# Kernel optimization log

Measured on AMD Instinct MI355X. Metric: run time of the kernel, lower is better.

## Reference

```python
import jax, jax.numpy as jnp
import numpy as np

B, S, H, NH, HD, L, I, M = 2, 2048, 768, 12, 64, 6, 3072, 256
VOCAB, TYPES = 30522, 2
EPS = 1e-6  # layernorm epsilon and FAVOR+ numerical stabilizer


def layer_norm(x, g, b):
    mu = jnp.mean(x, axis=-1, keepdims=True)
    var = jnp.mean(jax.lax.square(x), axis=-1, keepdims=True) - jax.lax.square(mu)
    return (x - mu) * jax.lax.rsqrt(var + EPS) * g + b


def favor_attention(q, k, v, mask, proj):
    # q,k,v: [B,S,NH,HD]; proj: [M,HD] random features; mask: [B,S] float
    dn = 1.0 / np.sqrt(np.sqrt(HD))      # data normalizer for softmax kernel
    ratio = 1.0 / np.sqrt(M)
    qn, kn = q * dn, k * dn
    qp = jnp.einsum('bsnd,md->bsnm', qn, proj)
    kp = jnp.einsum('bsnd,md->bsnm', kn, proj)
    qd = 0.5 * jnp.sum(qn * qn, axis=-1, keepdims=True)
    kd = 0.5 * jnp.sum(kn * kn, axis=-1, keepdims=True)
    # stabilizers: per-position max for queries, global (seq+feature) max for keys
    q_prime = ratio * (jnp.exp(qp - qd - jnp.max(qp, axis=-1, keepdims=True)) + EPS)
    k_prime = ratio * (jnp.exp(kp - kd - jnp.max(kp, axis=(1, 3), keepdims=True)) + EPS)
    k_prime = k_prime * mask[:, :, None, None]
    kv = jnp.einsum('bsnm,bsnd->bnmd', k_prime, v)          # [B,NH,M,HD]
    num = jnp.einsum('bsnm,bnmd->bsnd', q_prime, kv)        # [B,S,NH,HD]
    den = jnp.einsum('bsnm,bnm->bsn', q_prime, jnp.sum(k_prime, axis=1))
    return num / den[..., None]


def setup_inputs() -> dict:
    key = jax.random.key(0)
    ks = jax.random.split(key, 32)
    f = lambda i, shape, s=0.02: (jax.random.normal(ks[i], shape, jnp.float32) * s)
    inp = {
        'input_ids': jax.random.randint(ks[0], (B, S), 0, VOCAB, jnp.int32),
        'token_type_ids': jax.random.randint(ks[1], (B, S), 0, TYPES, jnp.int32),
        'position_ids': jnp.tile(jnp.arange(S, dtype=jnp.int32)[None, :], (B, 1)),
        'attention_mask': jnp.ones((B, S), jnp.int32),
        'word_emb': f(2, (VOCAB, H), 0.1),
        'pos_emb': f(3, (S, H), 0.1),
        'type_emb': f(4, (TYPES, H), 0.1),
        'emb_ln_g': jnp.ones((H,), jnp.float32),
        'emb_ln_b': jnp.zeros((H,), jnp.float32),
        'wq': f(5, (L, H, NH, HD)), 'bq': jnp.zeros((L, NH, HD), jnp.float32),
        'wk': f(6, (L, H, NH, HD)), 'bk': jnp.zeros((L, NH, HD), jnp.float32),
        'wv': f(7, (L, H, NH, HD)), 'bv': jnp.zeros((L, NH, HD), jnp.float32),
        'wo': f(8, (L, NH, HD, H)), 'bo': jnp.zeros((L, H), jnp.float32),
        'ln1_g': jnp.ones((L, H), jnp.float32), 'ln1_b': jnp.zeros((L, H), jnp.float32),
        'wi': f(9, (L, H, I)), 'bi': jnp.zeros((L, I), jnp.float32),
        'wo2': f(10, (L, I, H)), 'bo2': jnp.zeros((L, H), jnp.float32),
        'ln2_g': jnp.ones((L, H), jnp.float32), 'ln2_b': jnp.zeros((L, H), jnp.float32),
        'proj': jax.random.normal(ks[11], (L, M, HD), jnp.float32),
    }
    return inp


def reference(input_ids, token_type_ids, position_ids, attention_mask,
              word_emb, pos_emb, type_emb, emb_ln_g, emb_ln_b,
              wq, bq, wk, bk, wv, bv, wo, bo, ln1_g, ln1_b,
              wi, bi, wo2, bo2, ln2_g, ln2_b, proj):
    mask = attention_mask.astype(jnp.float32)
    x = word_emb[input_ids] + pos_emb[position_ids] + type_emb[token_type_ids]
    x = layer_norm(x, emb_ln_g, emb_ln_b)
    for l in range(L):
        q = jnp.einsum('bsh,hnd->bsnd', x, wq[l]) + bq[l]
        k = jnp.einsum('bsh,hnd->bsnd', x, wk[l]) + bk[l]
        v = jnp.einsum('bsh,hnd->bsnd', x, wv[l]) + bv[l]
        att = favor_attention(q, k, v, mask, proj[l])
        att = jnp.einsum('bsnd,ndh->bsh', att, wo[l]) + bo[l]
        a = layer_norm(att + x, ln1_g[l], ln1_b[l])
        inter = jax.nn.gelu(jnp.einsum('bsh,hi->bsi', a, wi[l]) + bi[l])
        out = jnp.einsum('bsi,ih->bsh', inter, wo2[l]) + bo2[l]
        x = layer_norm(out + a, ln2_g[l], ln2_b[l])
    return x
```

## Files before the change

kernel.cpp:

```cpp
#include <hip/hip_runtime.h>
#include <hip/hip_bf16.h>

#define B_ 2
#define S_ 2048
#define H_ 768
#define NH_ 12
#define HD_ 64
#define L_ 6
#define I_ 3072
#define M_ 256
#define BS_ 4096
#define R_ 49152
#define NXH_ 3145728
#define EPS_ 1e-6f
#define DN_ 0.35355339059327373f
#define RATIO_ 0.0625f

typedef __attribute__((ext_vector_type(8))) short bf16x8;
typedef __attribute__((ext_vector_type(4))) float f32x4;

__device__ __forceinline__ void gload16(const void* g, void* l) {
    __builtin_amdgcn_global_load_lds(
        (const __attribute__((address_space(1))) void*)g,
        (__attribute__((address_space(3))) void*)l, 16, 0, 0);
}

__device__ __forceinline__ float gelu_f(float x) {
    const float c = 0.7978845608028654f;
    float x3 = x * x * x;
    return 0.5f * x * (1.0f + tanhf(c * (x + 0.044715f * x3)));
}

__device__ __forceinline__ void blockReduceSum2(float& a, float& b) {
    __shared__ float sa[4], sb[4];
    int lane = threadIdx.x & 63, wid = threadIdx.x >> 6;
    #pragma unroll
    for (int off = 32; off; off >>= 1) {
        a += __shfl_down(a, off, 64);
        b += __shfl_down(b, off, 64);
    }
    __syncthreads();
    if (lane == 0) { sa[wid] = a; sb[wid] = b; }
    __syncthreads();
    a = sa[0] + sa[1] + sa[2] + sa[3];
    b = sb[0] + sb[1] + sb[2] + sb[3];
    __syncthreads();
}

__device__ __forceinline__ float blockReduceMax(float v) {
    __shared__ float sm[4];
    int lane = threadIdx.x & 63, wid = threadIdx.x >> 6;
    #pragma unroll
    for (int off = 32; off; off >>= 1) v = fmaxf(v, __shfl_down(v, off, 64));
    __syncthreads();
    if (lane == 0) sm[wid] = v;
    __syncthreads();
    float r = fmaxf(fmaxf(sm[0], sm[1]), fmaxf(sm[2], sm[3]));
    __syncthreads();
    return r;
}

__device__ __forceinline__ float blockReduceSum(float v) {
    __shared__ float sm[4];
    int lane = threadIdx.x & 63, wid = threadIdx.x >> 6;
    #pragma unroll
    for (int off = 32; off; off >>= 1) v += __shfl_down(v, off, 64);
    __syncthreads();
    if (lane == 0) sm[wid] = v;
    __syncthreads();
    float r = sm[0] + sm[1] + sm[2] + sm[3];
    __syncthreads();
    return r;
}

template<int ACT, int OUTMODE>
__global__ __launch_bounds__(256) void gemm_pipe3_kernel(
    const __hip_bfloat16* __restrict__ A, const __hip_bfloat16* __restrict__ BT,
    const float* __restrict__ bias, void* __restrict__ Cv,
    int K, int lda, int ldb, int ldc)
{
    __shared__ __align__(16) unsigned short As[3][128][32];
    __shared__ __align__(16) unsigned short Bs[3][128][32];
    const int tid = threadIdx.x, lane = tid & 63, wid = tid >> 6;
    const int wr = wid >> 1, wc = wid & 1;
    const size_t r0 = (size_t)blockIdx.y * 128;
    const int n0 = blockIdx.x * 128;

    const int srow = lane >> 2;
    const int selem = ((lane & 3) ^ ((srow >> 1) & 3)) * 8;
    const unsigned short* ga0 = (const unsigned short*)A + (r0 + wid * 32 + srow) * (size_t)lda + selem;
    const unsigned short* gb0 = (const unsigned short*)BT + ((size_t)n0 + wid * 32 + srow) * (size_t)ldb + selem;

    f32x4 acc[4][4];
    #pragma unroll
    for (int i = 0; i < 4; i++)
        #pragma unroll
        for (int j = 0; j < 4; j++)
            acc[i][j] = (f32x4){0.f, 0.f, 0.f, 0.f};

    const int lr = lane & 15;
    const int rc8 = (((lane >> 4) ^ ((lr >> 1) & 3))) * 8;

#define STAGE_(t) { const int bb_ = (t) % 3; const int kk_ = (t) * 32;            \
    gload16(ga0 + kk_, &As[bb_][wid * 32][0]);                                    \
    gload16(ga0 + kk_ + 16 * (size_t)lda, &As[bb_][wid * 32 + 16][0]);            \
    gload16(gb0 + kk_, &Bs[bb_][wid * 32][0]);                                    \
    gload16(gb0 + kk_ + 16 * (size_t)ldb, &Bs[bb_][wid * 32 + 16][0]); }

#define ITER_(t, VMSTR, DOSTAGE) {                                                \
    if (DOSTAGE) STAGE_((t) + 2);                                                 \
    asm volatile("s_waitcnt vmcnt(" VMSTR ")" ::: "memory");                      \
    __builtin_amdgcn_sched_barrier(0);                                            \
    __builtin_amdgcn_s_barrier();                                                 \
    __builtin_amdgcn_sched_barrier(0);                                            \
    const int bb_ = (t) % 3;                                                      \
    bf16x8 af[4], bfv[4];                                                         \
    _Pragma("unroll") for (int i = 0; i < 4; i++)                                 \
        af[i] = *(const bf16x8*)&As[bb_][wr * 64 + i * 16 + lr][rc8];             \
    _Pragma("unroll") for (int j = 0; j < 4; j++)                                 \
        bfv[j] = *(const bf16x8*)&Bs[bb_][wc * 64 + j * 16 + lr][rc8];            \
    __builtin_amdgcn_s_setprio(1);                                                \
    _Pragma("unroll") for (int i = 0; i < 4; i++)                                 \
        _Pragma("unroll") for (int j = 0; j < 4; j++)                             \
            acc[i][j] = __builtin_amdgcn_mfma_f32_16x16x32_bf16(af[i], bfv[j], acc[i][j], 0, 0, 0); \
    __builtin_amdgcn_s_setprio(0);                                                \
    __builtin_amdgcn_s_barrier();                                                 \
    __builtin_amdgcn_sched_barrier(0); }

    const int nT = K >> 5;
    STAGE_(0); STAGE_(1);
    for (int t = 0; t < nT - 2; ++t) ITER_(t, "8", true);
    ITER_(nT - 2, "4", false);
    ITER_(nT - 1, "0", false);
#undef ITER_
#undef STAGE_

    const int rr = (lane >> 4) * 4;
    const int cc = lane & 15;
    const size_t seg = (size_t)n0 / 768;
    const int colbase = n0 - (int)seg * 768;
    #pragma unroll
    for (int i = 0; i < 4; i++) {
        #pragma unroll
        for (int j = 0; j < 4; j++) {
            int colw = wc * 64 + j * 16 + cc;
            size_t col = (size_t)n0 + colw;
            float bv_ = bias ? bias[col] : 0.f;
            #pragma unroll
            for (int rg = 0; rg < 4; rg++) {
                size_t row = r0 + wr * 64 + i * 16 + rr + rg;
                float v = acc[i][j][rg] + bv_;
                if (ACT == 1) v = gelu_f(v);
                if (OUTMODE == 1)
                    ((__hip_bfloat16*)Cv)[row * (size_t)ldc + col] = __float2bfloat16(v);
                else
                    ((__hip_bfloat16*)Cv)[seg * (size_t)NXH_ + row * 768 + colbase + colw]
                        = __float2bfloat16(v);
            }
        }
    }
}

__global__ __launch_bounds__(256) void gemm_pipe3_n64_kernel(
    const __hip_bfloat16* __restrict__ A, const __hip_bfloat16* __restrict__ BT,
    const float* __restrict__ bias, float* __restrict__ C,
    int K, int lda, int ldb, int ldc)
{
    __shared__ __align__(16) unsigned short As[3][128][32];
    __shared__ __align__(16) unsigned short Bs[3][64][32];
    const int tid = threadIdx.x, lane = tid & 63, wid = tid >> 6;
    const size_t r0 = (size_t)blockIdx.y * 128;
    const int n0 = blockIdx.x * 64;

    const int srow = lane >> 2;
    const int selem = ((lane & 3) ^ ((srow >> 1) & 3)) * 8;
    const unsigned short* ga0 = (const unsigned short*)A + (r0 + wid * 32 + srow) * (size_t)lda + selem;
    const unsigned short* gb0 = (const unsigned short*)BT + ((size_t)n0 + wid * 16 + srow) * (size_t)ldb + selem;

    f32x4 acc[2][4];
    #pragma unroll
    for (int i = 0; i < 2; i++)
        #pragma unroll
        for (int j = 0; j < 4; j++)
            acc[i][j] = (f32x4){0.f, 0.f, 0.f, 0.f};

    const int lr = lane & 15;
    const int rc8 = (((lane >> 4) ^ ((lr >> 1) & 3))) * 8;

#define STAGE_(t) { const int bb_ = (t) % 3; const int kk_ = (t) * 32;            \
    gload16(ga0 + kk_, &As[bb_][wid * 32][0]);                                    \
    gload16(ga0 + kk_ + 16 * (size_t)lda, &As[bb_][wid * 32 + 16][0]);            \
    gload16(gb0 + kk_, &Bs[bb_][wid * 16][0]); }

#define ITER_(t, VMSTR, DOSTAGE) {                                                \
    if (DOSTAGE) STAGE_((t) + 2);                                                 \
    asm volatile("s_waitcnt vmcnt(" VMSTR ")" ::: "memory");                      \
    __builtin_amdgcn_sched_barrier(0);                                            \
    __builtin_amdgcn_s_barrier();                                                 \
    __builtin_amdgcn_sched_barrier(0);                                            \
    const int bb_ = (t) % 3;                                                      \
    bf16x8 af[2], bfv[4];                                                         \
    _Pragma("unroll") for (int i = 0; i < 2; i++)                                 \
        af[i] = *(const bf16x8*)&As[bb_][wid * 32 + i * 16 + lr][rc8];            \
    _Pragma("unroll") for (int j = 0; j < 4; j++)                                 \
        bfv[j] = *(const bf16x8*)&Bs[bb_][j * 16 + lr][rc8];                      \
    __builtin_amdgcn_s_setprio(1);                                                \
    _Pragma("unroll") for (int i = 0; i < 2; i++)                                 \
        _Pragma("unroll") for (int j = 0; j < 4; j++)                             \
            acc[i][j] = __builtin_amdgcn_mfma_f32_16x16x32_bf16(af[i], bfv[j], acc[i][j], 0, 0, 0); \
    __builtin_amdgcn_s_setprio(0);                                                \
    __builtin_amdgcn_s_barrier();                                                 \
    __builtin_amdgcn_sched_barrier(0); }

    const int nT = K >> 5;
    STAGE_(0); STAGE_(1);
    for (int t = 0; t < nT - 2; ++t) ITER_(t, "6", true);
    ITER_(nT - 2, "3", false);
    ITER_(nT - 1, "0", false);
#undef ITER_
#undef STAGE_

    const int rr = (lane >> 4) * 4, cc = lane & 15;
    #pragma unroll
    for (int i = 0; i < 2; i++) {
        #pragma unroll
        for (int j = 0; j < 4; j++) {
            int col = n0 + j * 16 + cc;
            float bv_ = bias ? bias[col] : 0.f;
            #pragma unroll
            for (int rg = 0; rg < 4; rg++) {
                size_t row = r0 + wid * 32 + i * 16 + rr + rg;
                C[row * (size_t)ldc + col] = acc[i][j][rg] + bv_;
            }
        }
    }
}

template<int RMAXOUT>
__global__ __launch_bounds__(256) void gemm_mfma_kernel(
    const __hip_bfloat16* __restrict__ A, const __hip_bfloat16* __restrict__ BT,
    void* __restrict__ Cv,
    int N, int K, int lda, int ldb, int ldc, float alpha,
    float* __restrict__ rmaxp)
{
    __shared__ __align__(16) unsigned short As[2][128][32];
    __shared__ __align__(16) unsigned short Bs[2][128][32];
    __shared__ float rmx[128][2];
    const int tid = threadIdx.x, lane = tid & 63, wid = tid >> 6;
    const int wr = wid >> 1, wc = wid & 1;
    const size_t r0 = (size_t)blockIdx.y * 128;
    const int n0 = blockIdx.x * 128;

    const int srow = lane >> 2;
    const int selem = ((lane & 3) ^ ((srow >> 1) & 3)) * 8;
    const unsigned short* ga0 = (const unsigned short*)A + (r0 + wid * 32 + srow) * (size_t)lda + selem;
    const unsigned short* gb0 = (const unsigned short*)BT + ((size_t)n0 + wid * 32 + srow) * (size_t)ldb + selem;

    f32x4 acc[4][4];
    #pragma unroll
    for (int i = 0; i < 4; i++)
        #pragma unroll
        for (int j = 0; j < 4; j++)
            acc[i][j] = (f32x4){0.f, 0.f, 0.f, 0.f};

    gload16(ga0, &As[0][wid * 32][0]);
    gload16(ga0 + 16 * (size_t)lda, &As[0][wid * 32 + 16][0]);
    gload16(gb0, &Bs[0][wid * 32][0]);
    gload16(gb0 + 16 * (size_t)ldb, &Bs[0][wid * 32 + 16][0]);
    __syncthreads();

    const int lr = lane & 15;
    const int rc8 = (((lane >> 4) ^ ((lr >> 1) & 3))) * 8;

    int cur = 0;
    for (int k0 = 0; k0 < K; k0 += 32) {
        const int kn = k0 + 32;
        if (kn < K) {
            gload16(ga0 + kn, &As[cur ^ 1][wid * 32][0]);
            gload16(ga0 + kn + 16 * (size_t)lda, &As[cur ^ 1][wid * 32 + 16][0]);
            gload16(gb0 + kn, &Bs[cur ^ 1][wid * 32][0]);
            gload16(gb0 + kn + 16 * (size_t)ldb, &Bs[cur ^ 1][wid * 32 + 16][0]);
        }
        bf16x8 af[4], bfv[4];
        #pragma unroll
        for (int i = 0; i < 4; i++)
            af[i] = *(const bf16x8*)&As[cur][wr * 64 + i * 16 + lr][rc8];
        #pragma unroll
        for (int j = 0; j < 4; j++)
            bfv[j] = *(const bf16x8*)&Bs[cur][wc * 64 + j * 16 + lr][rc8];
        #pragma unroll
        for (int i = 0; i < 4; i++)
            #pragma unroll
            for (int j = 0; j < 4; j++)
                acc[i][j] = __builtin_amdgcn_mfma_f32_16x16x32_bf16(af[i], bfv[j], acc[i][j], 0, 0, 0);
        __syncthreads();
        cur ^= 1;
    }

    const int rr = (lane >> 4) * 4;
    const int cc = lane & 15;
    #pragma unroll
    for (int i = 0; i < 4; i++) {
        #pragma unroll
        for (int j = 0; j < 4; j++) {
            int colw = wc * 64 + j * 16 + cc;
            size_t col = (size_t)n0 + colw;
            #pragma unroll
            for (int rg = 0; rg < 4; rg++) {
                size_t row = r0 + wr * 64 + i * 16 + rr + rg;
                ((float*)Cv)[row * ldc + col] = acc[i][j][rg] * alpha;
            }
        }
    }
    if (RMAXOUT) {
        #pragma unroll
        for (int i = 0; i < 4; i++) {
            #pragma unroll
            for (int rg = 0; rg < 4; rg++) {
                float rm = -3.4e38f;
                #pragma unroll
                for (int j = 0; j < 4; j++) rm = fmaxf(rm, acc[i][j][rg] * alpha);
                #pragma unroll
                for (int off = 1; off <= 8; off <<= 1)
                    rm = fmaxf(rm, __shfl_xor(rm, off, 64));
                if ((lane & 15) == 0) rmx[wr * 64 + i * 16 + rr + rg][wc] = rm;
            }
        }
        __syncthreads();
        if (tid < 128)
            rmaxp[(size_t)blockIdx.x * R_ + r0 + tid] = fmaxf(rmx[tid][0], rmx[tid][1]);
    }
}

__global__ __launch_bounds__(256) void num_mfma_kernel(
    const __hip_bfloat16* __restrict__ QPb, const __hip_bfloat16* __restrict__ kvT,
    const float* __restrict__ den, __hip_bfloat16* __restrict__ ATT)
{
    __shared__ __align__(16) unsigned short As[2][128][32];
    __shared__ __align__(16) unsigned short Bs[2][64][32];
    const int tid = threadIdx.x, lane = tid & 63, wid = tid >> 6;
    const int s0 = blockIdx.x * 128;
    const int bn = blockIdx.y, b = bn / NH_, n = bn % NH_;

    const int srow = lane >> 2;
    const int selem = ((lane & 3) ^ ((srow >> 1) & 3)) * 8;
    const unsigned short* ga0 = (const unsigned short*)QPb + (size_t)b * S_ * (NH_ * M_) + n * M_
                              + ((size_t)s0 + wid * 32 + srow) * (NH_ * M_) + selem;
    const unsigned short* gb0 = (const unsigned short*)kvT + (size_t)bn * (HD_ * M_)
                              + ((size_t)wid * 16 + srow) * M_ + selem;

    f32x4 acc[2][4];
    #pragma unroll
    for (int i = 0; i < 2; i++)
        #pragma unroll
        for (int j = 0; j < 4; j++)
            acc[i][j] = (f32x4){0.f, 0.f, 0.f, 0.f};

    gload16(ga0, &As[0][wid * 32][0]);
    gload16(ga0 + 16 * (size_t)(NH_ * M_), &As[0][wid * 32 + 16][0]);
    gload16(gb0, &Bs[0][wid * 16][0]);
    __syncthreads();

    const int lr = lane & 15;
    const int rc8 = (((lane >> 4) ^ ((lr >> 1) & 3))) * 8;

    int cur = 0;
    for (int k0 = 0; k0 < M_; k0 += 32) {
        const int kn = k0 + 32;
        if (kn < M_) {
            gload16(ga0 + kn, &As[cur ^ 1][wid * 32][0]);
            gload16(ga0 + kn + 16 * (size_t)(NH_ * M_), &As[cur ^ 1][wid * 32 + 16][0]);
            gload16(gb0 + kn, &Bs[cur ^ 1][wid * 16][0]);
        }
        bf16x8 af[2], bfv[4];
        #pragma unroll
        for (int i = 0; i < 2; i++)
            af[i] = *(const bf16x8*)&As[cur][wid * 32 + i * 16 + lr][rc8];
        #pragma unroll
        for (int j = 0; j < 4; j++)
            bfv[j] = *(const bf16x8*)&Bs[cur][j * 16 + lr][rc8];
        #pragma unroll
        for (int i = 0; i < 2; i++)
            #pragma unroll
            for (int j = 0; j < 4; j++)
                acc[i][j] = __builtin_amdgcn_mfma_f32_16x16x32_bf16(af[i], bfv[j], acc[i][j], 0, 0, 0);
        __syncthreads();
        cur ^= 1;
    }

    const int rr = (lane >> 4) * 4, cc = lane & 15;
    #pragma unroll
    for (int i = 0; i < 2; i++) {
        #pragma unroll
        for (int rg = 0; rg < 4; rg++) {
            int s = s0 + wid * 32 + i * 16 + rr + rg;
            float inv = 1.0f / den[((size_t)b * S_ + s) * NH_ + n];
            #pragma unroll
            for (int j = 0; j < 4; j++)
                ATT[((size_t)b * S_ + s) * H_ + n * HD_ + j * 16 + cc]
                    = __float2bfloat16(acc[i][j][rg] * inv);
        }
    }
}

__global__ __launch_bounds__(256) void kv_splitk_kernel(
    const float* __restrict__ KP, const __hip_bfloat16* __restrict__ Vb, float* __restrict__ part)
{
    const int m0 = blockIdx.x * 64, bn = blockIdx.y, b = bn / NH_, n = bn % NH_;
    const int s0 = blockIdx.z * 256;
    __shared__ __align__(16) float As2[16][68];
    __shared__ __align__(16) float Bs2[16][68];
    const int tid = threadIdx.x, tx = tid & 15, ty = tid >> 4;
    float acc[4][4] = {};
    for (int ss = 0; ss < 256; ss += 16) {
        #pragma unroll
        for (int i = 0; i < 4; i++) {
            int idx = tid + i * 256;
            int kk = idx >> 6, c = idx & 63;
            size_t srow = (size_t)b * S_ + s0 + ss + kk;
            As2[kk][c] = KP[srow * (NH_ * M_) + n * M_ + m0 + c];
            Bs2[kk][c] = __bfloat162float(Vb[srow * H_ + n * HD_ + c]);
        }
        __syncthreads();
        #pragma unroll
        for (int kk = 0; kk < 16; kk++) {
            float4 av = *reinterpret_cast<const float4*>(&As2[kk][ty * 4]);
            float4 bv = *reinterpret_cast<const float4*>(&Bs2[kk][tx * 4]);
            float a4[4] = {av.x, av.y, av.z, av.w};
            float b4[4] = {bv.x, bv.y, bv.z, bv.w};
            #pragma unroll
            for (int i = 0; i < 4; i++)
                #pragma unroll
                for (int j = 0; j < 4; j++)
                    acc[i][j] += a4[i] * b4[j];
        }
        __syncthreads();
    }
    float* Cb = part + ((size_t)blockIdx.z * (B_ * NH_) + bn) * (M_ * HD_);
    #pragma unroll
    for (int i = 0; i < 4; i++)
        #pragma unroll
        for (int j = 0; j < 4; j++)
            Cb[(size_t)(m0 + ty * 4 + i) * HD_ + tx * 4 + j] = acc[i][j];
}

__global__ __launch_bounds__(256) void kvred_kernel(
    const float* __restrict__ part, __hip_bfloat16* __restrict__ kvT)
{
    const int bn = blockIdx.x, m = threadIdx.x;
    for (int d = 0; d < HD_; d++) {
        float s = 0.f;
        #pragma unroll
        for (int c = 0; c < 8; c++)
            s += part[((size_t)c * (B_ * NH_) + bn) * (M_ * HD_) + (size_t)m * HD_ + d];
        kvT[(size_t)bn * (HD_ * M_) + (size_t)d * M_ + m] = __float2bfloat16(s);
    }
}

__global__ __launch_bounds__(256) void prep_kernel(
    const float* __restrict__ wq_l, const float* __restrict__ wk_l,
    const float* __restrict__ wv_l, const float* __restrict__ wo_l,
    const float* __restrict__ wi_l, const float* __restrict__ wo2_l,
    const float* __restrict__ proj_l,
    const float* __restrict__ bq_l, const float* __restrict__ bk_l, const float* __restrict__ bv_l,
    __hip_bfloat16* __restrict__ wqT, __hip_bfloat16* __restrict__ wkT,
    __hip_bfloat16* __restrict__ wvT, __hip_bfloat16* __restrict__ woT,
    __hip_bfloat16* __restrict__ wiT, __hip_bfloat16* __restrict__ wo2T,
    __hip_bfloat16* __restrict__ projb, float* __restrict__ biasq)
{
    __shared__ float tile[32][33];
    int bid = blockIdx.x;
    if (bid < 6912) {
        const float* src; __hip_bfloat16* dst; int K, N, kt, nt;
        if (bid < 2304) {
            int t = bid / 576, idx = bid % 576;
            src = (t == 0) ? wq_l : (t == 1) ? wk_l : (t == 2) ? wv_l : wo_l;
            dst = (t == 0) ? wqT : (t == 1) ? wkT : (t == 2) ? wvT : woT;
            K = 768; N = 768; kt = idx % 24; nt = idx / 24;
        } else if (bid < 4608) {
            int idx = bid - 2304;
            src = wi_l; dst = wiT; K = 768; N = 3072;
            kt = idx % 24; nt = idx / 24;
        } else {
            int idx = bid - 4608;
            src = wo2_l; dst = wo2T; K = 3072; N = 768;
            kt = idx % 96; nt = idx / 96;
        }
        int k0 = kt * 32, n0 = nt * 32;
        int tx = threadIdx.x & 31, ty = threadIdx.x >> 5;
        #pragma unroll
        for (int i = 0; i < 4; i++)
            tile[ty + i * 8][tx] = src[(size_t)(k0 + ty + i * 8) * N + n0 + tx];
        __syncthreads();
        #pragma unroll
        for (int i = 0; i < 4; i++)
            dst[(size_t)(n0 + ty + i * 8) * K + k0 + tx] = __float2bfloat16(tile[tx][ty + i * 8]);
    } else if (bid < 6976) {
        int i = (bid - 6912) * 256 + threadIdx.x;
        projb[i] = __float2bfloat16(proj_l[i]);
    } else {
        int i = (bid - 6976) * 256 + threadIdx.x;
        if (i < 768) biasq[i] = bq_l[i];
        else if (i < 1536) biasq[i] = bk_l[i - 768];
        else if (i < 2304) biasq[i] = bv_l[i - 1536];
    }
}

__global__ __launch_bounds__(256) void embed_ln_kernel(
    const int* __restrict__ ids, const int* __restrict__ tts, const int* __restrict__ pos,
    const float* __restrict__ wemb, const float* __restrict__ pemb, const float* __restrict__ temb,
    const float* __restrict__ g, const float* __restrict__ bb,
    float* __restrict__ out, __hip_bfloat16* __restrict__ outb)
{
    size_t row = blockIdx.x;
    int id = ids[row], tt = tts[row], ps = pos[row];
    const float* w0 = wemb + (size_t)id * H_;
    const float* p0 = pemb + (size_t)ps * H_;
    const float* t0 = temb + (size_t)tt * H_;
    float vals[3], s1 = 0.f, s2 = 0.f;
    #pragma unroll
    for (int i = 0; i < 3; i++) {
        int h = threadIdx.x + i * 256;
        float v = w0[h] + p0[h] + t0[h];
        vals[i] = v; s1 += v; s2 += v * v;
    }
    blockReduceSum2(s1, s2);
    float mu = s1 * (1.0f / H_);
    float var = s2 * (1.0f / H_) - mu * mu;
    float rs = rsqrtf(var + EPS_);
    #pragma unroll
    for (int i = 0; i < 3; i++) {
        int h = threadIdx.x + i * 256;
        float y = (vals[i] - mu) * rs * g[h] + bb[h];
        out[row * H_ + h] = y;
        outb[row * H_ + h] = __float2bfloat16(y);
    }
}

__global__ __launch_bounds__(256) void add_ln_kernel(
    const float* __restrict__ P, const float* __restrict__ Q,
    const float* __restrict__ g, const float* __restrict__ bb,
    float* __restrict__ out, __hip_bfloat16* __restrict__ outb)
{
    size_t row = blockIdx.x;
    float vals[3], s1 = 0.f, s2 = 0.f;
    #pragma unroll
    for (int i = 0; i < 3; i++) {
        int h = threadIdx.x + i * 256;
        float v = P[row * H_ + h] + Q[row * H_ + h];
        vals[i] = v; s1 += v; s2 += v * v;
    }
    blockReduceSum2(s1, s2);
    float mu = s1 * (1.0f / H_);
    float var = s2 * (1.0f / H_) - mu * mu;
    float rs = rsqrtf(var + EPS_);
    #pragma unroll
    for (int i = 0; i < 3; i++) {
        int h = threadIdx.x + i * 256;
        float y = (vals[i] - mu) * rs * g[h] + bb[h];
        out[row * H_ + h] = y;
        if (outb) outb[row * H_ + h] = __float2bfloat16(y);
    }
}

__global__ __launch_bounds__(256) void rowsq_bf16_kernel(
    const __hip_bfloat16* __restrict__ X, float* __restrict__ out, float scale)
{
    int lane = threadIdx.x & 63, wid = threadIdx.x >> 6;
    size_t r = (size_t)blockIdx.x * 4 + wid;
    float v = __bfloat162float(X[r * 64 + lane]);
    float s = v * v;
    #pragma unroll
    for (int off = 32; off; off >>= 1) s += __shfl_down(s, off, 64);
    if (lane == 0) out[r] = scale * s;
}

__global__ __launch_bounds__(256) void gmax_kernel(
    const float* __restrict__ rmaxp, float* __restrict__ gmax)
{
    int bn = blockIdx.x, b = bn / NH_, n = bn % NH_;
    float mx = -3.4e38f;
    for (int s = threadIdx.x; s < S_; s += 256) {
        size_t r = ((size_t)b * S_ + s) * NH_ + n;
        mx = fmaxf(mx, fmaxf(rmaxp[r], rmaxp[R_ + r]));
    }
    mx = blockReduceMax(mx);
    if (threadIdx.x == 0) gmax[bn] = mx;
}

__global__ __launch_bounds__(256) void kprime_ksum_kernel(
    float* __restrict__ KP, const float* __restrict__ kd,
    const float* __restrict__ gmax, const int* __restrict__ amask,
    float* __restrict__ kpart)
{
    const int bn = blockIdx.x, chunk = blockIdx.y;
    const int b = bn / NH_, n = bn % NH_;
    const int m = threadIdx.x;
    const float gm = gmax[bn];
    float acc = 0.f;
    for (int si = 0; si < 64; si++) {
        size_t bs = (size_t)b * S_ + chunk * 64 + si;
        size_t r = bs * NH_ + n;
        float mk = (float)amask[bs];
        size_t e = r * M_ + m;
        float v = RATIO_ * (expf(KP[e] - kd[r] - gm) + EPS_) * mk;
        KP[e] = v;
        acc += v;
    }
    kpart[((size_t)bn * 32 + chunk) * M_ + m] = acc;
}

__global__ __launch_bounds__(256) void ksum_final_kernel(
    const float* __restrict__ part, float* __restrict__ ksum)
{
    int bn = blockIdx.x, m = threadIdx.x;
    float s = 0.f;
    #pragma unroll
    for (int c = 0; c < 32; c++) s += part[((size_t)bn * 32 + c) * M_ + m];
    ksum[(size_t)bn * M_ + m] = s;
}

__global__ __launch_bounds__(256) void qprime_den_kernel(
    const float* __restrict__ QP, const float* __restrict__ qd,
    const float* __restrict__ ksum, const float* __restrict__ rmaxp,
    float* __restrict__ den, __hip_bfloat16* __restrict__ QPb)
{
    size_t r = blockIdx.x;
    int n = (int)(r % NH_);
    int b = (int)(r / ((size_t)S_ * NH_));
    int bn = b * NH_ + n;
    float mx = fmaxf(rmaxp[r], rmaxp[R_ + r]);
    float v = QP[r * M_ + threadIdx.x];
    float qp = RATIO_ * (expf(v - qd[r] - mx) + EPS_);
    __hip_bfloat16 qb = __float2bfloat16(qp);
    QPb[r * M_ + threadIdx.x] = qb;
    float qpr = __bfloat162float(qb);
    float d = blockReduceSum(qpr * ksum[(size_t)bn * M_ + threadIdx.x]);
    if (threadIdx.x == 0) den[r] = d;
}

extern "C" void kernel_launch(void* const* d_in, const int* in_sizes, int n_in,
                              void* d_out, int out_size, void* d_ws, size_t ws_size,
                              hipStream_t stream)
{
    const int* input_ids  = (const int*)d_in[0];
    const int* token_type = (const int*)d_in[1];
    const int* position   = (const int*)d_in[2];
    const int* amask      = (const int*)d_in[3];
    const float* wemb = (const float*)d_in[4];
    const float* pemb = (const float*)d_in[5];
    const float* temb = (const float*)d_in[6];
    const float* elng = (const float*)d_in[7];
    const float* elnb = (const float*)d_in[8];
    const float* wq  = (const float*)d_in[9];
    const float* bq  = (const float*)d_in[10];
    const float* wk  = (const float*)d_in[11];
    const float* bk  = (const float*)d_in[12];
    const float* wv  = (const float*)d_in[13];
    const float* bv  = (const float*)d_in[14];
    const float* wo  = (const float*)d_in[15];
    const float* bo  = (const float*)d_in[16];
    const float* ln1g = (const float*)d_in[17];
    const float* ln1b = (const float*)d_in[18];
    const float* wi  = (const float*)d_in[19];
    const float* bi  = (const float*)d_in[20];
    const float* wo2 = (const float*)d_in[21];
    const float* bo2 = (const float*)d_in[22];
    const float* ln2g = (const float*)d_in[23];
    const float* ln2b = (const float*)d_in[24];
    const float* proj = (const float*)d_in[25];

    float* ws = (float*)d_ws;
    float* X    = ws;
    float* T2   = X + 3145728;
    float* BIG  = T2 + 3145728;
    float* U    = BIG + 12582912;
    __hip_bfloat16* Xb  = (__hip_bfloat16*)(U + 6291456);
    __hip_bfloat16* Qb  = (__hip_bfloat16*)((float*)Xb + 1572864);
    __hip_bfloat16* Kb  = Qb + 3145728;
    __hip_bfloat16* Vb  = Kb + 3145728;
    __hip_bfloat16* BF1 = Vb + 3145728;
    __hip_bfloat16* WT  = BF1 + 3145728;
    float* kvT_f = (float*)(WT + 7094272);
    __hip_bfloat16* kvT = (__hip_bfloat16*)kvT_f;
    float* KSUM  = kvT_f + 196608;
    float* KPART = KSUM + 6144;
    float* RMAXP = KPART + 196608;
    float* GMAX  = RMAXP + 98304;
    float* QD    = GMAX + 64;
    float* KD    = QD + 49152;
    float* DEN   = KD + 49152;
    float* BIASQ = DEN + 49152;
    float* T1    = (float*)d_out;

    __hip_bfloat16* wqT  = WT;
    __hip_bfloat16* wkT  = wqT + 589824;
    __hip_bfloat16* wvT  = wkT + 589824;
    __hip_bfloat16* woT  = wvT + 589824;
    __hip_bfloat16* wiT  = woT + 589824;
    __hip_bfloat16* wo2T = wiT + 2359296;
    __hip_bfloat16* projb = wo2T + 2359296;
    __hip_bfloat16* QPb = (__hip_bfloat16*)U;
    float* PART = U;
    __hip_bfloat16* BIGb = (__hip_bfloat16*)BIG;

    embed_ln_kernel<<<BS_, 256, 0, stream>>>(input_ids, token_type, position,
        wemb, pemb, temb, elng, elnb, X, Xb);

    const float sqscale = 0.5f * DN_ * DN_;
    for (int l = 0; l < L_; l++) {
        const float* wq_l = wq + (size_t)l * H_ * NH_ * HD_;
        const float* wk_l = wk + (size_t)l * H_ * NH_ * HD_;
        const float* wv_l = wv + (size_t)l * H_ * NH_ * HD_;
        const float* wo_l = wo + (size_t)l * NH_ * HD_ * H_;
        const float* bq_l = bq + (size_t)l * NH_ * HD_;
        const float* bk_l = bk + (size_t)l * NH_ * HD_;
        const float* bv_l = bv + (size_t)l * NH_ * HD_;
        const float* bo_l = bo + (size_t)l * H_;
        const float* wi_l = wi + (size_t)l * H_ * I_;
        const float* bi_l = bi + (size_t)l * I_;
        const float* wo2_l = wo2 + (size_t)l * I_ * H_;
        const float* bo2_l = bo2 + (size_t)l * H_;
        const float* proj_l = proj + (size_t)l * M_ * HD_;

        prep_kernel<<<6985, 256, 0, stream>>>(wq_l, wk_l, wv_l, wo_l, wi_l, wo2_l, proj_l,
            bq_l, bk_l, bv_l, wqT, wkT, wvT, woT, wiT, wo2T, projb, BIASQ);

        gemm_pipe3_kernel<0,2><<<dim3(18,32), 256, 0, stream>>>(
            Xb, wqT, BIASQ, (void*)Qb, 768, 768, 768, 768);

        rowsq_bf16_kernel<<<2*R_/4, 256, 0, stream>>>(Qb, QD, sqscale);

        gemm_mfma_kernel<1><<<dim3(2,384), 256, 0, stream>>>(
            Kb, projb, BIG, 256, 64, 64, 64, 256, DN_, RMAXP);
        gmax_kernel<<<B_*NH_, 256, 0, stream>>>(RMAXP, GMAX);
        kprime_ksum_kernel<<<dim3(B_*NH_, 32), 256, 0, stream>>>(BIG, KD, GMAX, amask, KPART);
        ksum_final_kernel<<<B_*NH_, 256, 0, stream>>>(KPART, KSUM);
        kv_splitk_kernel<<<dim3(4, B_*NH_, 8), 256, 0, stream>>>(BIG, Vb, PART);
        kvred_kernel<<<B_*NH_, 256, 0, stream>>>(PART, kvT);

        gemm_mfma_kernel<1><<<dim3(2,384), 256, 0, stream>>>(
            Qb, projb, BIG, 256, 64, 64, 64, 256, DN_, RMAXP);
        qprime_den_kernel<<<R_, 256, 0, stream>>>(BIG, QD, KSUM, RMAXP, DEN, QPb);
        num_mfma_kernel<<<dim3(16, B_*NH_), 256, 0, stream>>>(QPb, kvT, DEN, BF1);

        gemm_pipe3_n64_kernel<<<dim3(12,32), 256, 0, stream>>>(
            BF1, woT, bo_l, T1, 768, 768, 768, 768);
        add_ln_kernel<<<BS_, 256, 0, stream>>>(T1, X, ln1g + (size_t)l*H_, ln1b + (size_t)l*H_, T2, BF1);

        gemm_pipe3_kernel<1,1><<<dim3(24,32), 256, 0, stream>>>(
            BF1, wiT, bi_l, (void*)BIGb, 768, 768, 768, 3072);

        gemm_pipe3_n64_kernel<<<dim3(12,32), 256, 0, stream>>>(
            BIGb, wo2T, bo2_l, T1, 3072, 3072, 3072, 768);
        float* xout = (l == L_ - 1) ? (float*)d_out : X;
        add_ln_kernel<<<BS_, 256, 0, stream>>>(T1, T2, ln2g + (size_t)l*H_, ln2b + (size_t)l*H_, xout, Xb);
    }
}
```

Measured before the change: 1.898 ms.

## Fuse Q/K row norms into QKV GEMM and Q-projection with denominator, store K' in bf16

The QKV GEMM epilogue now computes the per-head squared norms for Q and K, which removes the separate rowsq kernel. The Q random-feature projection, row max, exp, q' bf16 store and denominator dot product are fused into one 512-thread kernel, replacing a fp32 QP round trip and the per-row qprime_den kernel. The K projection now writes bf16 instead of fp32, halving traffic through the k' and kv stages. The cost is lower precision in kp/k' and more register and LDS pressure in the fused epilogues.

Result: no change. 1.881 ms (-0.9%).

```diff
diff --git a/kernel.cpp b/kernel.cpp
--- a/kernel.cpp
+++ b/kernel.cpp
@@ -60,24 +60,11 @@
     return r;
 }
 
-__device__ __forceinline__ float blockReduceSum(float v) {
-    __shared__ float sm[4];
-    int lane = threadIdx.x & 63, wid = threadIdx.x >> 6;
-    #pragma unroll
-    for (int off = 32; off; off >>= 1) v += __shfl_down(v, off, 64);
-    __syncthreads();
-    if (lane == 0) sm[wid] = v;
-    __syncthreads();
-    float r = sm[0] + sm[1] + sm[2] + sm[3];
-    __syncthreads();
-    return r;
-}
-
 template<int ACT, int OUTMODE>
 __global__ __launch_bounds__(256) void gemm_pipe3_kernel(
     const __hip_bfloat16* __restrict__ A, const __hip_bfloat16* __restrict__ BT,
     const float* __restrict__ bias, void* __restrict__ Cv,
-    int K, int lda, int ldb, int ldc)
+    int K, int lda, int ldb, int ldc, float* __restrict__ qdkd)
 {
     __shared__ __align__(16) unsigned short As[3][128][32];
     __shared__ __align__(16) unsigned short Bs[3][128][32];
@@ -142,20 +129,34 @@
     #pragma unroll
     for (int i = 0; i < 4; i++) {
         #pragma unroll
-        for (int j = 0; j < 4; j++) {
-            int colw = wc * 64 + j * 16 + cc;
-            size_t col = (size_t)n0 + colw;
-            float bv_ = bias ? bias[col] : 0.f;
-            #pragma unroll
-            for (int rg = 0; rg < 4; rg++) {
-                size_t row = r0 + wr * 64 + i * 16 + rr + rg;
+        for (int rg = 0; rg < 4; rg++) {
+            size_t row = r0 + wr * 64 + i * 16 + rr + rg;
+            float ss = 0.f;
+            #pragma unroll
+            for (int j = 0; j < 4; j++) {
+                int colw = wc * 64 + j * 16 + cc;
+                size_t col = (size_t)n0 + colw;
+                float bv_ = bias ? bias[col] : 0.f;
                 float v = acc[i][j][rg] + bv_;
                 if (ACT == 1) v = gelu_f(v);
+                __hip_bfloat16 hb = __float2bfloat16(v);
                 if (OUTMODE == 1)
-                    ((__hip_bfloat16*)Cv)[row * (size_t)ldc + col] = __float2bfloat16(v);
+                    ((__hip_bfloat16*)Cv)[row * (size_t)ldc + col] = hb;
                 else
-                    ((__hip_bfloat16*)Cv)[seg * (size_t)NXH_ + row * 768 + colbase + colw]
-                        = __float2bfloat16(v);
+                    ((__hip_bfloat16*)Cv)[seg * (size_t)NXH_ + row * 768 + colbase + colw] = hb;
+                if (OUTMODE == 2) {
+                    float vr = __bfloat162float(hb);
+                    ss += vr * vr;
+                }
+            }
+            if (OUTMODE == 2) {
+                #pragma unroll
+                for (int off = 1; off <= 8; off <<= 1)
+                    ss += __shfl_xor(ss, off, 64);
+                if (seg < 2 && (lane & 15) == 0) {
+                    int nh = colbase / 64 + wc;
+                    qdkd[seg * (size_t)R_ + row * 12 + nh] = 0.5f * DN_ * DN_ * ss;
+                }
             }
         }
     }
@@ -236,11 +237,10 @@
     }
 }
 
-template<int RMAXOUT>
-__global__ __launch_bounds__(256) void gemm_mfma_kernel(
+__global__ __launch_bounds__(256) void gemm_projk_kernel(
     const __hip_bfloat16* __restrict__ A, const __hip_bfloat16* __restrict__ BT,
-    void* __restrict__ Cv,
-    int N, int K, int lda, int ldb, int ldc, float alpha,
+    __hip_bfloat16* __restrict__ Cv,
+    int K, int lda, int ldb, int ldc, float alpha,
     float* __restrict__ rmaxp)
 {
     __shared__ __align__(16) unsigned short As[2][128][32];
@@ -308,28 +308,135 @@
             #pragma unroll
             for (int rg = 0; rg < 4; rg++) {
                 size_t row = r0 + wr * 64 + i * 16 + rr + rg;
-                ((float*)Cv)[row * ldc + col] = acc[i][j][rg] * alpha;
+                Cv[row * ldc + col] = __float2bfloat16(acc[i][j][rg] * alpha);
             }
         }
     }
-    if (RMAXOUT) {
-        #pragma unroll
-        for (int i = 0; i < 4; i++) {
-            #pragma unroll
-            for (int rg = 0; rg < 4; rg++) {
-                float rm = -3.4e38f;
-                #pragma unroll
-                for (int j = 0; j < 4; j++) rm = fmaxf(rm, acc[i][j][rg] * alpha);
-                #pragma unroll
-                for (int off = 1; off <= 8; off <<= 1)
-                    rm = fmaxf(rm, __shfl_xor(rm, off, 64));
-                if ((lane & 15) == 0) rmx[wr * 64 + i * 16 + rr + rg][wc] = rm;
+    #pragma unroll
+    for (int i = 0; i < 4; i++) {
+        #pragma unroll
+        for (int rg = 0; rg < 4; rg++) {
+            float rm = -3.4e38f;
+            #pragma unroll
+            for (int j = 0; j < 4; j++) rm = fmaxf(rm, acc[i][j][rg] * alpha);
+            #pragma unroll
+            for (int off = 1; off <= 8; off <<= 1)
+                rm = fmaxf(rm, __shfl_xor(rm, off, 64));
+            if ((lane & 15) == 0) rmx[wr * 64 + i * 16 + rr + rg][wc] = rm;
+        }
+    }
+    __syncthreads();
+    if (tid < 128)
+        rmaxp[(size_t)blockIdx.x * R_ + r0 + tid] = fmaxf(rmx[tid][0], rmx[tid][1]);
+}
+
+__global__ __launch_bounds__(512) void projq_den_kernel(
+    const __hip_bfloat16* __restrict__ Qbp, const __hip_bfloat16* __restrict__ projb,
+    const float* __restrict__ qd, const float* __restrict__ ksum,
+    __hip_bfloat16* __restrict__ QPb, float* __restrict__ den)
+{
+    __shared__ __align__(16) unsigned short Asm[128][64];
+    __shared__ __align__(16) unsigned short Bsm[256][64];
+    __shared__ float ksl[12][256];
+    __shared__ float red[128][4];
+    __shared__ float rmaxv[128];
+    __shared__ float qdl[128];
+    const int tid = threadIdx.x, lane = tid & 63, w = tid >> 6;
+    const int wrow = w >> 2, wcol = w & 3;
+    const size_t r0 = (size_t)blockIdx.x * 128;
+    const int b = (int)(r0 / 24576);
+
+    #pragma unroll
+    for (int it = 0; it < 6; it++) {
+        int idx = tid + it * 512;
+        ksl[idx >> 8][idx & 255] = ksum[((size_t)b * 12 + (idx >> 8)) * 256 + (idx & 255)];
+    }
+    if (tid < 128) qdl[tid] = qd[r0 + tid];
+
+    const int lrow = lane >> 3, lch = lane & 7;
+    const int sch = (lch ^ (lrow & 7)) * 8;
+    #pragma unroll
+    for (int it = 0; it < 2; it++) {
+        int segr = (w * 2 + it) * 8;
+        gload16((const unsigned short*)Qbp + (r0 + segr + lrow) * 64 + sch, &Asm[segr][0]);
+    }
+    #pragma unroll
+    for (int it = 0; it < 4; it++) {
+        int segr = (w * 4 + it) * 8;
+        gload16((const unsigned short*)projb + (size_t)(segr + lrow) * 64 + sch, &Bsm[segr][0]);
+    }
+    __syncthreads();
+
+    const int lr = lane & 15, kq = lane >> 4;
+    f32x4 acc[4][4];
+    #pragma unroll
+    for (int i = 0; i < 4; i++)
+        #pragma unroll
+        for (int j = 0; j < 4; j++)
+            acc[i][j] = (f32x4){0.f, 0.f, 0.f, 0.f};
+
+    #pragma unroll
+    for (int ks = 0; ks < 2; ks++) {
+        const int ch = (((ks << 2) | kq) ^ (lr & 7)) * 8;
+        bf16x8 af[4], bfv[4];
+        #pragma unroll
+        for (int i = 0; i < 4; i++)
+            af[i] = *(const bf16x8*)&Asm[wrow * 64 + i * 16 + lr][ch];
+        #pragma unroll
+        for (int j = 0; j < 4; j++)
+            bfv[j] = *(const bf16x8*)&Bsm[wcol * 64 + j * 16 + lr][ch];
+        #pragma unroll
+        for (int i = 0; i < 4; i++)
+            #pragma unroll
+            for (int j = 0; j < 4; j++)
+                acc[i][j] = __builtin_amdgcn_mfma_f32_16x16x32_bf16(af[i], bfv[j], acc[i][j], 0, 0, 0);
+    }
+
+    #pragma unroll
+    for (int i = 0; i < 4; i++) {
+        #pragma unroll
+        for (int rg = 0; rg < 4; rg++) {
+            float rm = -3.4e38f;
+            #pragma unroll
+            for (int j = 0; j < 4; j++) rm = fmaxf(rm, acc[i][j][rg] * DN_);
+            #pragma unroll
+            for (int off = 1; off <= 8; off <<= 1)
+                rm = fmaxf(rm, __shfl_xor(rm, off, 64));
+            if ((lane & 15) == 0) red[wrow * 64 + i * 16 + kq * 4 + rg][wcol] = rm;
+        }
+    }
+    __syncthreads();
+    if (tid < 128)
+        rmaxv[tid] = fmaxf(fmaxf(red[tid][0], red[tid][1]), fmaxf(red[tid][2], red[tid][3]));
+    __syncthreads();
+
+    #pragma unroll
+    for (int i = 0; i < 4; i++) {
+        #pragma unroll
+        for (int rg = 0; rg < 4; rg++) {
+            int row = wrow * 64 + i * 16 + kq * 4 + rg;
+            size_t rglob = r0 + row;
+            int nh = (int)(rglob % 12);
+            float qdv = qdl[row], mx = rmaxv[row];
+            float dsum = 0.f;
+            #pragma unroll
+            for (int j = 0; j < 4; j++) {
+                int col = wcol * 64 + j * 16 + lr;
+                float qp = acc[i][j][rg] * DN_;
+                float qv = RATIO_ * (expf(qp - qdv - mx) + EPS_);
+                __hip_bfloat16 qb = __float2bfloat16(qv);
+                QPb[rglob * 256 + col] = qb;
+                dsum += __bfloat162float(qb) * ksl[nh][col];
             }
-        }
-        __syncthreads();
-        if (tid < 128)
-            rmaxp[(size_t)blockIdx.x * R_ + r0 + tid] = fmaxf(rmx[tid][0], rmx[tid][1]);
-    }
+            #pragma unroll
+            for (int off = 1; off <= 8; off <<= 1)
+                dsum += __shfl_xor(dsum, off, 64);
+            if ((lane & 15) == 0) red[row][wcol] = dsum;
+        }
+    }
+    __syncthreads();
+    if (tid < 128)
+        den[r0 + tid] = red[tid][0] + red[tid][1] + red[tid][2] + red[tid][3];
 }
 
 __global__ __launch_bounds__(256) void num_mfma_kernel(
@@ -404,7 +511,8 @@
 }
 
 __global__ __launch_bounds__(256) void kv_splitk_kernel(
-    const float* __restrict__ KP, const __hip_bfloat16* __restrict__ Vb, float* __restrict__ part)
+    const __hip_bfloat16* __restrict__ KPb, const __hip_bfloat16* __restrict__ Vb,
+    float* __restrict__ part)
 {
     const int m0 = blockIdx.x * 64, bn = blockIdx.y, b = bn / NH_, n = bn % NH_;
     const int s0 = blockIdx.z * 256;
@@ -418,7 +526,7 @@
             int idx = tid + i * 256;
             int kk = idx >> 6, c = idx & 63;
             size_t srow = (size_t)b * S_ + s0 + ss + kk;
-            As2[kk][c] = KP[srow * (NH_ * M_) + n * M_ + m0 + c];
+            As2[kk][c] = __bfloat162float(KPb[srow * (NH_ * M_) + n * M_ + m0 + c]);
             Bs2[kk][c] = __bfloat162float(Vb[srow * H_ + n * HD_ + c]);
         }
         __syncthreads();
@@ -563,18 +671,6 @@
     }
 }
 
-__global__ __launch_bounds__(256) void rowsq_bf16_kernel(
-    const __hip_bfloat16* __restrict__ X, float* __restrict__ out, float scale)
-{
-    int lane = threadIdx.x & 63, wid = threadIdx.x >> 6;
-    size_t r = (size_t)blockIdx.x * 4 + wid;
-    float v = __bfloat162float(X[r * 64 + lane]);
-    float s = v * v;
-    #pragma unroll
-    for (int off = 32; off; off >>= 1) s += __shfl_down(s, off, 64);
-    if (lane == 0) out[r] = scale * s;
-}
-
 __global__ __launch_bounds__(256) void gmax_kernel(
     const float* __restrict__ rmaxp, float* __restrict__ gmax)
 {
@@ -589,7 +685,7 @@
 }
 
 __global__ __launch_bounds__(256) void kprime_ksum_kernel(
-    float* __restrict__ KP, const float* __restrict__ kd,
+    __hip_bfloat16* __restrict__ KPb, const float* __restrict__ kd,
     const float* __restrict__ gmax, const int* __restrict__ amask,
     float* __restrict__ kpart)
 {
@@ -603,9 +699,10 @@
         size_t r = bs * NH_ + n;
         float mk = (float)amask[bs];
         size_t e = r * M_ + m;
-        float v = RATIO_ * (expf(KP[e] - kd[r] - gm) + EPS_) * mk;
-        KP[e] = v;
-        acc += v;
+        float v = RATIO_ * (expf(__bfloat162float(KPb[e]) - kd[r] - gm) + EPS_) * mk;
+        __hip_bfloat16 hb = __float2bfloat16(v);
+        KPb[e] = hb;
+        acc += __bfloat162float(hb);
     }
     kpart[((size_t)bn * 32 + chunk) * M_ + m] = acc;
 }
@@ -618,25 +715,6 @@
     #pragma unroll
     for (int c = 0; c < 32; c++) s += part[((size_t)bn * 32 + c) * M_ + m];
     ksum[(size_t)bn * M_ + m] = s;
-}
-
-__global__ __launch_bounds__(256) void qprime_den_kernel(
-    const float* __restrict__ QP, const float* __restrict__ qd,
-    const float* __restrict__ ksum, const float* __restrict__ rmaxp,
-    float* __restrict__ den, __hip_bfloat16* __restrict__ QPb)
-{
-    size_t r = blockIdx.x;
-    int n = (int)(r % NH_);
-    int b = (int)(r / ((size_t)S_ * NH_));
-    int bn = b * NH_ + n;
-    float mx = fmaxf(rmaxp[r], rmaxp[R_ + r]);
-    float v = QP[r * M_ + threadIdx.x];
-    float qp = RATIO_ * (expf(v - qd[r] - mx) + EPS_);
-    __hip_bfloat16 qb = __float2bfloat16(qp);
-    QPb[r * M_ + threadIdx.x] = qb;
-    float qpr = __bfloat162float(qb);
-    float d = blockReduceSum(qpr * ksum[(size_t)bn * M_ + threadIdx.x]);
-    if (threadIdx.x == 0) den[r] = d;
 }
 
 extern "C" void kernel_launch(void* const* d_in, const int* in_sizes, int n_in,
@@ -707,7 +785,6 @@
     embed_ln_kernel<<<BS_, 256, 0, stream>>>(input_ids, token_type, position,
         wemb, pemb, temb, elng, elnb, X, Xb);
 
-    const float sqscale = 0.5f * DN_ * DN_;
     for (int l = 0; l < L_; l++) {
         const float* wq_l = wq + (size_t)l * H_ * NH_ * HD_;
         const float* wk_l = wk + (size_t)l * H_ * NH_ * HD_;
@@ -727,21 +804,17 @@
             bq_l, bk_l, bv_l, wqT, wkT, wvT, woT, wiT, wo2T, projb, BIASQ);
 
         gemm_pipe3_kernel<0,2><<<dim3(18,32), 256, 0, stream>>>(
-            Xb, wqT, BIASQ, (void*)Qb, 768, 768, 768, 768);
-
-        rowsq_bf16_kernel<<<2*R_/4, 256, 0, stream>>>(Qb, QD, sqscale);
-
-        gemm_mfma_kernel<1><<<dim3(2,384), 256, 0, stream>>>(
-            Kb, projb, BIG, 256, 64, 64, 64, 256, DN_, RMAXP);
+            Xb, wqT, BIASQ, (void*)Qb, 768, 768, 768, 768, QD);
+
+        gemm_projk_kernel<<<dim3(2,384), 256, 0, stream>>>(
+            Kb, projb, BIGb, 64, 64, 64, 256, DN_, RMAXP);
         gmax_kernel<<<B_*NH_, 256, 0, stream>>>(RMAXP, GMAX);
-        kprime_ksum_kernel<<<dim3(B_*NH_, 32), 256, 0, stream>>>(BIG, KD, GMAX, amask, KPART);
+        kprime_ksum_kernel<<<dim3(B_*NH_, 32), 256, 0, stream>>>(BIGb, KD, GMAX, amask, KPART);
         ksum_final_kernel<<<B_*NH_, 256, 0, stream>>>(KPART, KSUM);
-        kv_splitk_kernel<<<dim3(4, B_*NH_, 8), 256, 0, stream>>>(BIG, Vb, PART);
+        kv_splitk_kernel<<<dim3(4, B_*NH_, 8), 256, 0, stream>>>(BIGb, Vb, PART);
         kvred_kernel<<<B_*NH_, 256, 0, stream>>>(PART, kvT);
 
-        gemm_mfma_kernel<1><<<dim3(2,384), 256, 0, stream>>>(
-            Qb, projb, BIG, 256, 64, 64, 64, 256, DN_, RMAXP);
-        qprime_den_kernel<<<R_, 256, 0, stream>>>(BIG, QD, KSUM, RMAXP, DEN, QPb);
+        projq_den_kernel<<<384, 512, 0, stream>>>(Qb, projb, QD, KSUM, QPb, DEN);
         num_mfma_kernel<<<dim3(16, B_*NH_), 256, 0, stream>>>(QPb, kvT, DEN, BF1);
 
         gemm_pipe3_n64_kernel<<<dim3(12,32), 256, 0, stream>>>(
@@ -749,7 +822,7 @@
         add_ln_kernel<<<BS_, 256, 0, stream>>>(T1, X, ln1g + (size_t)l*H_, ln1b + (size_t)l*H_, T2, BF1);
 
         gemm_pipe3_kernel<1,1><<<dim3(24,32), 256, 0, stream>>>(
-            BF1, wiT, bi_l, (void*)BIGb, 768, 768, 768, 3072);
+            BF1, wiT, bi_l, (void*)BIGb, 768, 768, 768, 3072, nullptr);
 
         gemm_pipe3_n64_kernel<<<dim3(12,32), 256, 0, stream>>>(
             BIGb, wo2T, bo2_l, T1, 3072, 3072, 3072, 768);
```
